# Optimization experiments

Hardware: AMD Instinct MI355X
Metric: run time of the kernel (lower is better)

Reference implementation:

```python
import jax, jax.numpy as jnp
import numpy as np

N_NODES = 50000
N_EDGES = 800000
IN_DIM = 32
HID = 64
OUT_DIM = 4
HEADS = 4
LAYERS = 3
N_GRAPHS = 50
NEG_SLOPE = 0.2
BN_EPS = 1e-5


def setup_inputs() -> dict:
    key = jax.random.key(0)
    ks = jax.random.split(key, 20)
    x = jax.random.normal(ks[0], (N_NODES, IN_DIM), dtype=jnp.float32)
    edge_index = jax.random.randint(ks[1], (2, N_EDGES), 0, N_NODES, dtype=jnp.int64)
    batch = jnp.sort(jax.random.randint(ks[2], (N_NODES,), 0, N_GRAPHS, dtype=jnp.int64))
    s = 0.05
    inp = {
        "x": x,
        "edge_index": edge_index,
        "batch": batch,
        "in_W": jax.random.normal(ks[3], (IN_DIM, HID), jnp.float32) * s,
        "in_b": jnp.zeros((HID,), jnp.float32),
        "gat_W": jax.random.normal(ks[4], (LAYERS, HID, HEADS * HID), jnp.float32) * s,
        "att_src": jax.random.normal(ks[5], (LAYERS, HEADS, HID), jnp.float32) * s,
        "att_dst": jax.random.normal(ks[6], (LAYERS, HEADS, HID), jnp.float32) * s,
        "gat_b": jnp.zeros((LAYERS, HID), jnp.float32),
        "bn_g": jnp.ones((LAYERS, HID), jnp.float32),
        "bn_b": jnp.zeros((LAYERS, HID), jnp.float32),
        "bn_m": jnp.zeros((LAYERS, HID), jnp.float32),
        "bn_v": jnp.ones((LAYERS, HID), jnp.float32),
        "fc1_W": jax.random.normal(ks[7], (HID, HID), jnp.float32) * s,
        "fc1_b": jnp.zeros((HID,), jnp.float32),
        "fc2_W": jax.random.normal(ks[8], (HID, OUT_DIM), jnp.float32) * s,
        "fc2_b": jnp.zeros((OUT_DIM,), jnp.float32),
    }
    return inp


def _gat_layer(x, src, dst, W, a_src, a_dst, b):
    # x: [N, HID]; src/dst: [E'] (self-loops included)
    N = x.shape[0]
    xt = (x @ W).reshape(N, HEADS, HID)           # [N, H, C]
    sc_src = jnp.einsum("nhc,hc->nh", xt, a_src)  # [N, H]
    sc_dst = jnp.einsum("nhc,hc->nh", xt, a_dst)
    e = jax.nn.leaky_relu(sc_src[src] + sc_dst[dst], NEG_SLOPE)  # [E, H]
    # segment softmax over incoming edges of each dst node
    emax = jax.ops.segment_max(e, dst, num_segments=N)
    ex = jnp.exp(e - emax[dst])
    denom = jax.ops.segment_sum(ex, dst, num_segments=N)
    alpha = ex / (denom[dst] + 1e-16)             # [E, H]
    msg = xt[src] * alpha[:, :, None]             # [E, H, C]
    out = jax.ops.segment_sum(msg, dst, num_segments=N)  # [N, H, C]
    return out.mean(axis=1) + b                   # head-average (concat=False)


def reference(x, edge_index, batch, in_W, in_b, gat_W, att_src, att_dst, gat_b,
              bn_g, bn_b, bn_m, bn_v, fc1_W, fc1_b, fc2_W, fc2_b):
    N = x.shape[0]
    loops = jnp.arange(N, dtype=edge_index.dtype)
    src = jnp.concatenate([edge_index[0], loops])
    dst = jnp.concatenate([edge_index[1], loops])

    h = x @ in_W + in_b  # dropout: eval mode (identity)
    for i in range(LAYERS):
        identity = h
        h = _gat_layer(h, src, dst, gat_W[i], att_src[i], att_dst[i], gat_b[i])
        # BatchNorm1d in eval mode (running stats)
        h = (h - bn_m[i]) * jax.lax.rsqrt(bn_v[i] + BN_EPS) * bn_g[i] + bn_b[i]
        h = jax.nn.relu(h)
        h = h + identity

    # global mean pool over graphs
    sums = jax.ops.segment_sum(h, batch, num_segments=N_GRAPHS)
    cnt = jax.ops.segment_sum(jnp.ones((N,), h.dtype), batch, num_segments=N_GRAPHS)
    g = sums / jnp.maximum(cnt, 1.0)[:, None]     # [N_GRAPHS, HID]

    g = jax.nn.relu(g @ fc1_W + fc1_b)
    return g @ fc2_W + fc2_b                      # [N_GRAPHS, OUT_DIM]
```

## Files before the change

### kernel.cpp

```cpp
#include <hip/hip_runtime.h>
#include <hip/hip_fp16.h>
#include <math.h>

#define HID 64
#define HEADS 4
#define HC 256
#define IN_DIM 32
#define NEG 0.2f
#define BN_EPS 1e-5f
#define CAP 64

typedef _Float16 f16;
typedef _Float16 f16x8 __attribute__((ext_vector_type(8)));
typedef float f32x4 __attribute__((ext_vector_type(4)));

__device__ __forceinline__ int ld_idx(const int* __restrict__ p, int i, int f64) {
    return f64 ? p[(size_t)2 * i] : p[i];
}

__global__ void k_init(const int* __restrict__ ei, int* __restrict__ flag,
                       int* __restrict__ deg, float* __restrict__ gsum,
                       int N, int NG) {
    int i = blockIdx.x * blockDim.x + threadIdx.x;
    if (i == 0) {
        int z = 1;
#pragma unroll
        for (int k = 1; k < 64; k += 2) z &= (ei[k] == 0);
        *flag = z;
    }
    if (i < N) deg[i] = 0;
    if (i < NG) gsum[i] = 0.f;
}

__global__ void k_build(const int* __restrict__ ei, const int* __restrict__ flagp,
                        int* __restrict__ deg, unsigned short* __restrict__ src_pad,
                        int E) {
    int e = blockIdx.x * blockDim.x + threadIdx.x;
    if (e >= E) return;
    const int f = *flagp;
    int s = ld_idx(ei, e, f);
    int d = ld_idx(ei, E + e, f);
    int pos = atomicAdd(&deg[d], 1);
    if (pos < CAP) src_pad[(size_t)d * CAP + pos] = (unsigned short)s;
}

__global__ void k_wtilde(const float* __restrict__ gat_W, const float* __restrict__ asrc,
                         const float* __restrict__ adst, float* __restrict__ wts,
                         float* __restrict__ wtd) {
    int l = blockIdx.x;
    int t = threadIdx.x;
    int hh = t >> 6, k = t & 63;
    const float* W = gat_W + (size_t)l * HID * HC + (size_t)k * HC + hh * HID;
    const float* as = asrc + (size_t)l * HEADS * HID + hh * HID;
    const float* ad = adst + (size_t)l * HEADS * HID + hh * HID;
    float s1 = 0.f, s2 = 0.f;
#pragma unroll
    for (int c = 0; c < HID; ++c) { s1 += W[c] * as[c]; s2 += W[c] * ad[c]; }
    wts[l * HC + hh * HID + k] = s1;
    wtd[l * HC + hh * HID + k] = s2;
}

__global__ void k_prepB(const float* __restrict__ gat_W, __half* __restrict__ BT) {
    int l = blockIdx.x;
    int t = threadIdx.x;
    int c = t & 63, jg = t >> 6;
    const float* W = gat_W + (size_t)l * HID * HC;
    __half* o = BT + (size_t)l * HID * HC + (size_t)c * HC + jg * 64;
#pragma unroll
    for (int jj = 0; jj < 64; ++jj)
        o[jj] = __float2half(W[(size_t)jj * HC + jg * 64 + c]);
}

__global__ __launch_bounds__(256) void k_input(
        const float* __restrict__ x, const float* __restrict__ W,
        const float* __restrict__ b, const float* __restrict__ wts0,
        const float* __restrict__ wtd0, float* __restrict__ h,
        __half* __restrict__ h16, float* __restrict__ ssrc,
        float* __restrict__ sdst, int N) {
    int w = threadIdx.x >> 6, lane = threadIdx.x & 63;
    int n = blockIdx.x * 4 + w;
    if (n >= N) return;
    float xv = x[(size_t)n * IN_DIM + (lane & 31)];
    float acc = b[lane];
#pragma unroll
    for (int k = 0; k < IN_DIM; ++k)
        acc += __shfl(xv, k, 64) * W[k * HID + lane];
    h[(size_t)n * HID + lane] = acc;
    h16[(size_t)n * HID + lane] = __float2half(acc);
    float p0 = acc * wts0[0 * HID + lane];
    float p1 = acc * wts0[1 * HID + lane];
    float p2 = acc * wts0[2 * HID + lane];
    float p3 = acc * wts0[3 * HID + lane];
    float q0 = acc * wtd0[0 * HID + lane];
    float q1 = acc * wtd0[1 * HID + lane];
    float q2 = acc * wtd0[2 * HID + lane];
    float q3 = acc * wtd0[3 * HID + lane];
#pragma unroll
    for (int m = 32; m >= 1; m >>= 1) {
        p0 += __shfl_xor(p0, m, 64); p1 += __shfl_xor(p1, m, 64);
        p2 += __shfl_xor(p2, m, 64); p3 += __shfl_xor(p3, m, 64);
        q0 += __shfl_xor(q0, m, 64); q1 += __shfl_xor(q1, m, 64);
        q2 += __shfl_xor(q2, m, 64); q3 += __shfl_xor(q3, m, 64);
    }
    if (lane == 0) {
        *(float4*)(ssrc + (size_t)n * HEADS) = make_float4(p0, p1, p2, p3);
        *(float4*)(sdst + (size_t)n * HEADS) = make_float4(q0, q1, q2, q3);
    }
}

__global__ __launch_bounds__(256) void k_gather(
        const int* __restrict__ deg, const unsigned short* __restrict__ src_pad,
        const float* __restrict__ ssrc, const float* __restrict__ sdst,
        const __half* __restrict__ h16, __half* __restrict__ agg, int N) {
    int d = blockIdx.x * 4 + (threadIdx.x >> 6);
    if (d >= N) return;
    const int lane = threadIdx.x & 63;
    const int g = lane >> 4, l16 = lane & 15;
    const int dg = min(deg[d], CAP);
    const int se = (int)src_pad[(size_t)d * CAP + lane];
    const float4 sdd = *(const float4*)(sdst + (size_t)d * HEADS);
    float den0 = 0.f, den1 = 0.f, den2 = 0.f, den3 = 0.f;
    float a00=0.f,a01=0.f,a02=0.f,a03=0.f, a10=0.f,a11=0.f,a12=0.f,a13=0.f;
    float a20=0.f,a21=0.f,a22=0.f,a23=0.f, a30=0.f,a31=0.f,a32=0.f,a33=0.f;
    {
        float4 ssd = *(const float4*)(ssrc + (size_t)d * HEADS);
        uint2 hu = *(const uint2*)(h16 + (size_t)d * HID + l16 * 4);
        float2 f01 = __half22float2(*(__half2*)&hu.x);
        float2 f23 = __half22float2(*(__half2*)&hu.y);
        if (g == 0) {
            float v0 = ssd.x + sdd.x; v0 = v0 > 0.f ? v0 : NEG * v0;
            float v1 = ssd.y + sdd.y; v1 = v1 > 0.f ? v1 : NEG * v1;
            float v2 = ssd.z + sdd.z; v2 = v2 > 0.f ? v2 : NEG * v2;
            float v3 = ssd.w + sdd.w; v3 = v3 > 0.f ? v3 : NEG * v3;
            float e0 = __expf(v0), e1 = __expf(v1), e2 = __expf(v2), e3 = __expf(v3);
            den0 = e0; den1 = e1; den2 = e2; den3 = e3;
            a00 = e0*f01.x; a01 = e0*f01.y; a02 = e0*f23.x; a03 = e0*f23.y;
            a10 = e1*f01.x; a11 = e1*f01.y; a12 = e1*f23.x; a13 = e1*f23.y;
            a20 = e2*f01.x; a21 = e2*f01.y; a22 = e2*f23.x; a23 = e2*f23.y;
            a30 = e3*f01.x; a31 = e3*f01.y; a32 = e3*f23.x; a33 = e3*f23.y;
        }
    }
    for (int b = 0; b < dg; b += 4) {
        int idx = b + g;
        bool valid = idx < dg;
        int s = __shfl(se, idx, 64);
        s = valid ? s : d;
        float4 ss = *(const float4*)(ssrc + (size_t)s * HEADS);
        uint2 hu = *(const uint2*)(h16 + (size_t)s * HID + l16 * 4);
        float u0 = ss.x + sdd.x; u0 = u0 > 0.f ? u0 : NEG * u0;
        float u1 = ss.y + sdd.y; u1 = u1 > 0.f ? u1 : NEG * u1;
        float u2 = ss.z + sdd.z; u2 = u2 > 0.f ? u2 : NEG * u2;
        float u3 = ss.w + sdd.w; u3 = u3 > 0.f ? u3 : NEG * u3;
        float e0 = valid ? __expf(u0) : 0.f;
        float e1 = valid ? __expf(u1) : 0.f;
        float e2 = valid ? __expf(u2) : 0.f;
        float e3 = valid ? __expf(u3) : 0.f;
        float2 f01 = __half22float2(*(__half2*)&hu.x);
        float2 f23 = __half22float2(*(__half2*)&hu.y);
        den0 += e0; den1 += e1; den2 += e2; den3 += e3;
        a00 += e0*f01.x; a01 += e0*f01.y; a02 += e0*f23.x; a03 += e0*f23.y;
        a10 += e1*f01.x; a11 += e1*f01.y; a12 += e1*f23.x; a13 += e1*f23.y;
        a20 += e2*f01.x; a21 += e2*f01.y; a22 += e2*f23.x; a23 += e2*f23.y;
        a30 += e3*f01.x; a31 += e3*f01.y; a32 += e3*f23.x; a33 += e3*f23.y;
    }
#define FOLD(v) { v += __shfl_xor(v, 16, 64); v += __shfl_xor(v, 32, 64); }
    FOLD(den0) FOLD(den1) FOLD(den2) FOLD(den3)
    FOLD(a00) FOLD(a01) FOLD(a02) FOLD(a03)
    FOLD(a10) FOLD(a11) FOLD(a12) FOLD(a13)
    FOLD(a20) FOLD(a21) FOLD(a22) FOLD(a23)
    FOLD(a30) FOLD(a31) FOLD(a32) FOLD(a33)
#undef FOLD
    float iv, o0, o1, o2, o3;
    if (g == 0)      { iv = 0.25f / den0; o0 = a00; o1 = a01; o2 = a02; o3 = a03; }
    else if (g == 1) { iv = 0.25f / den1; o0 = a10; o1 = a11; o2 = a12; o3 = a13; }
    else if (g == 2) { iv = 0.25f / den2; o0 = a20; o1 = a21; o2 = a22; o3 = a23; }
    else             { iv = 0.25f / den3; o0 = a30; o1 = a31; o2 = a32; o3 = a33; }
    __half2 q01 = __floats2half2_rn(o0 * iv, o1 * iv);
    __half2 q23 = __floats2half2_rn(o2 * iv, o3 * iv);
    uint2 st;
    st.x = *(unsigned int*)&q01;
    st.y = *(unsigned int*)&q23;
    *(uint2*)(agg + ((size_t)d * HC + g * HID + l16 * 4)) = st;
}

__global__ __launch_bounds__(256) void k_postW(
        const __half* __restrict__ agg, const __half* __restrict__ BT,
        const float* __restrict__ gb, const float* __restrict__ bg,
        const float* __restrict__ bb, const float* __restrict__ bm,
        const float* __restrict__ bv, const float* __restrict__ wtsn,
        const float* __restrict__ wtdn, float* __restrict__ h,
        __half* __restrict__ h16, float* __restrict__ ssrc,
        float* __restrict__ sdst, int N) {
    __shared__ float lds[64][68];
    const int t = threadIdx.x;
    const int w = t >> 6, l = t & 63;
    const int l16 = l & 15, lk = l >> 4;
    const f16* BTf = (const f16*)BT;
    const f16* af = (const f16*)agg;
    f16x8 bf[8][4];
#pragma unroll
    for (int ks = 0; ks < 8; ++ks)
#pragma unroll
        for (int nt = 0; nt < 4; ++nt)
            bf[ks][nt] = *(const f16x8*)(BTf + (size_t)(nt * 16 + l16) * HC + ks * 32 + lk * 8);
    int row = blockIdx.x * 64 + w * 16 + l16;
    int rowc = min(row, N - 1);
    f32x4 acc[4];
#pragma unroll
    for (int nt = 0; nt < 4; ++nt) acc[nt] = (f32x4){0.f, 0.f, 0.f, 0.f};
#pragma unroll
    for (int ks = 0; ks < 8; ++ks) {
        f16x8 a = *(const f16x8*)(af + (size_t)rowc * HC + ks * 32 + lk * 8);
#pragma unroll
        for (int nt = 0; nt < 4; ++nt)
            acc[nt] = __builtin_amdgcn_mfma_f32_16x16x32_f16(a, bf[ks][nt], acc[nt], 0, 0, 0);
    }
#pragma unroll
    for (int nt = 0; nt < 4; ++nt)
#pragma unroll
        for (int r = 0; r < 4; ++r)
            lds[w * 16 + lk * 4 + r][nt * 16 + l16] = acc[nt][r];
    __syncthreads();
    {
        int j = t >> 2, q = t & 3;
        int n = blockIdx.x * 64 + j;
        if (n < N) {
            int c0 = q * 16;
            float o[16];
            float* hrow = h + (size_t)n * HID;
#pragma unroll
            for (int i4 = 0; i4 < 4; ++i4) {
                int c = c0 + i4 * 4;
                float4 sv = *(const float4*)&lds[j][c];
                float4 r4 = *(const float4*)(hrow + c);
                float4 gb4 = *(const float4*)(gb + c);
                float4 bg4 = *(const float4*)(bg + c);
                float4 bb4 = *(const float4*)(bb + c);
                float4 bm4 = *(const float4*)(bm + c);
                float4 bv4 = *(const float4*)(bv + c);
                float4 ov;
                float v;
                v = sv.x + gb4.x; v = (v - bm4.x) * rsqrtf(bv4.x + BN_EPS) * bg4.x + bb4.x;
                ov.x = fmaxf(v, 0.f) + r4.x;
                v = sv.y + gb4.y; v = (v - bm4.y) * rsqrtf(bv4.y + BN_EPS) * bg4.y + bb4.y;
                ov.y = fmaxf(v, 0.f) + r4.y;
                v = sv.z + gb4.z; v = (v - bm4.z) * rsqrtf(bv4.z + BN_EPS) * bg4.z + bb4.z;
                ov.z = fmaxf(v, 0.f) + r4.z;
                v = sv.w + gb4.w; v = (v - bm4.w) * rsqrtf(bv4.w + BN_EPS) * bg4.w + bb4.w;
                ov.w = fmaxf(v, 0.f) + r4.w;
                *(float4*)(hrow + c) = ov;
                o[i4 * 4 + 0] = ov.x; o[i4 * 4 + 1] = ov.y;
                o[i4 * 4 + 2] = ov.z; o[i4 * 4 + 3] = ov.w;
            }
            {
                __half2 hp[8];
#pragma unroll
                for (int i = 0; i < 8; ++i)
                    hp[i] = __floats2half2_rn(o[2 * i], o[2 * i + 1]);
                uint4 u0, u1;
                u0.x = *(unsigned*)&hp[0]; u0.y = *(unsigned*)&hp[1];
                u0.z = *(unsigned*)&hp[2]; u0.w = *(unsigned*)&hp[3];
                u1.x = *(unsigned*)&hp[4]; u1.y = *(unsigned*)&hp[5];
                u1.z = *(unsigned*)&hp[6]; u1.w = *(unsigned*)&hp[7];
                *(uint4*)(h16 + (size_t)n * HID + c0) = u0;
                *(uint4*)(h16 + (size_t)n * HID + c0 + 8) = u1;
            }
            if (wtsn) {
                float ps0 = 0.f, ps1 = 0.f, ps2 = 0.f, ps3 = 0.f;
                float pd0 = 0.f, pd1 = 0.f, pd2 = 0.f, pd3 = 0.f;
#pragma unroll
                for (int i = 0; i < 16; ++i) {
                    int c = c0 + i;
                    float ov = o[i];
                    ps0 += ov * wtsn[0 * HID + c]; ps1 += ov * wtsn[1 * HID + c];
                    ps2 += ov * wtsn[2 * HID + c]; ps3 += ov * wtsn[3 * HID + c];
                    pd0 += ov * wtdn[0 * HID + c]; pd1 += ov * wtdn[1 * HID + c];
                    pd2 += ov * wtdn[2 * HID + c]; pd3 += ov * wtdn[3 * HID + c];
                }
#pragma unroll
                for (int m = 2; m >= 1; m >>= 1) {
                    ps0 += __shfl_xor(ps0, m, 64); ps1 += __shfl_xor(ps1, m, 64);
                    ps2 += __shfl_xor(ps2, m, 64); ps3 += __shfl_xor(ps3, m, 64);
                    pd0 += __shfl_xor(pd0, m, 64); pd1 += __shfl_xor(pd1, m, 64);
                    pd2 += __shfl_xor(pd2, m, 64); pd3 += __shfl_xor(pd3, m, 64);
                }
                if (q == 0) {
                    *(float4*)(ssrc + (size_t)n * HEADS) = make_float4(ps0, ps1, ps2, ps3);
                    *(float4*)(sdst + (size_t)n * HEADS) = make_float4(pd0, pd1, pd2, pd3);
                }
            }
        }
    }
}

#define NPBK 64
__global__ void k_pool_sum(const float* __restrict__ h, const int* __restrict__ batch,
                           const int* __restrict__ flagp, float* __restrict__ gsum, int N) {
    const int f = *flagp;
    int c = threadIdx.x;
    int n0 = blockIdx.x * NPBK;
    int n1 = min(n0 + NPBK, N);
    if (n0 >= N) return;
    int cur = ld_idx(batch, n0, f);
    float s = 0.f;
    for (int n = n0; n < n1; ++n) {
        int g = ld_idx(batch, n, f);
        if (g != cur) {
            atomicAdd(&gsum[cur * HID + c], s);
            s = 0.f;
            cur = g;
        }
        s += h[(size_t)n * HID + c];
    }
    atomicAdd(&gsum[cur * HID + c], s);
}

__device__ __forceinline__ int lower_bound_i(const int* __restrict__ a, int n, int v, int f) {
    int lo = 0, hi = n;
    while (lo < hi) {
        int mid = (lo + hi) >> 1;
        if (ld_idx(a, mid, f) < v) lo = mid + 1; else hi = mid;
    }
    return lo;
}

__global__ void k_mlp(const float* __restrict__ gsum, const int* __restrict__ batch,
                      const int* __restrict__ flagp, int N,
                      const float* __restrict__ W1, const float* __restrict__ b1,
                      const float* __restrict__ W2, const float* __restrict__ b2,
                      float* __restrict__ out, int OUTD) {
    int gg = blockIdx.x, c = threadIdx.x;
    const int f = *flagp;
    int lo = lower_bound_i(batch, N, gg, f);
    int hi = lower_bound_i(batch, N, gg + 1, f);
    float cnt = (float)(hi - lo);
    __shared__ float gs[HID];
    __shared__ float s1[HID];
    gs[c] = gsum[gg * HID + c] / fmaxf(cnt, 1.f);
    __syncthreads();
    float acc = b1[c];
#pragma unroll
    for (int k = 0; k < HID; ++k) acc += gs[k] * W1[k * HID + c];
    s1[c] = fmaxf(acc, 0.f);
    __syncthreads();
    if (c < OUTD) {
        float o = b2[c];
#pragma unroll
        for (int k = 0; k < HID; ++k) o += s1[k] * W2[k * OUTD + c];
        out[gg * OUTD + c] = o;
    }
}

extern "C" void kernel_launch(void* const* d_in, const int* in_sizes, int n_in,
                              void* d_out, int out_size, void* d_ws, size_t ws_size,
                              hipStream_t stream) {
    const float* x       = (const float*)d_in[0];
    const int*   ei_raw  = (const int*)d_in[1];
    const int*   b_raw   = (const int*)d_in[2];
    const float* in_W    = (const float*)d_in[3];
    const float* in_b    = (const float*)d_in[4];
    const float* gat_W   = (const float*)d_in[5];
    const float* att_src = (const float*)d_in[6];
    const float* att_dst = (const float*)d_in[7];
    const float* gat_b   = (const float*)d_in[8];
    const float* bn_g    = (const float*)d_in[9];
    const float* bn_b    = (const float*)d_in[10];
    const float* bn_m    = (const float*)d_in[11];
    const float* bn_v    = (const float*)d_in[12];
    const float* fc1_W   = (const float*)d_in[13];
    const float* fc1_b   = (const float*)d_in[14];
    const float* fc2_W   = (const float*)d_in[15];
    const float* fc2_b   = (const float*)d_in[16];

    const int N = in_sizes[2];
    const int E = in_sizes[1] / 2;
    const int OUTD = 4;
    const int G = out_size / OUTD;

    float*  h    = (float*)d_ws;
    __half* h16  = (__half*)(h + (size_t)N * HID);
    __half* agg  = h16 + (size_t)N * HID;
    float*  ssrc = (float*)(agg + (size_t)N * HC);
    float*  sdst = ssrc + (size_t)N * HEADS;
    float*  wts  = sdst + (size_t)N * HEADS;
    float*  wtd  = wts + 3 * HC;
    __half* BT   = (__half*)(wtd + 3 * HC);
    float*  gsum = (float*)(BT + 3 * HID * HC);
    int*    deg  = (int*)(gsum + (size_t)G * HID);
    unsigned short* src_pad = (unsigned short*)(deg + N);
    int*    flag = (int*)(src_pad + (size_t)N * CAP);

    k_init<<<(max(N, G * HID) + 255) / 256, 256, 0, stream>>>(
        ei_raw, flag, deg, gsum, N, G * HID);
    k_build<<<(E + 255) / 256, 256, 0, stream>>>(ei_raw, flag, deg, src_pad, E);
    k_wtilde<<<3, 256, 0, stream>>>(gat_W, att_src, att_dst, wts, wtd);
    k_prepB<<<3, 256, 0, stream>>>(gat_W, BT);
    k_input<<<(N + 3) / 4, 256, 0, stream>>>(x, in_W, in_b, wts, wtd, h, h16,
                                             ssrc, sdst, N);

    for (int l = 0; l < 3; ++l) {
        k_gather<<<(N + 3) / 4, 256, 0, stream>>>(
            deg, src_pad, ssrc, sdst, h16, agg, N);
        const float* wtsn = (l < 2) ? (wts + (l + 1) * HC) : nullptr;
        const float* wtdn = (l < 2) ? (wtd + (l + 1) * HC) : nullptr;
        k_postW<<<(N + 63) / 64, 256, 0, stream>>>(
            agg, BT + (size_t)l * HID * HC,
            gat_b + (size_t)l * HID, bn_g + (size_t)l * HID, bn_b + (size_t)l * HID,
            bn_m + (size_t)l * HID, bn_v + (size_t)l * HID,
            wtsn, wtdn, h, h16, ssrc, sdst, N);
    }

    k_pool_sum<<<(N + NPBK - 1) / NPBK, HID, 0, stream>>>(h, b_raw, flag, gsum, N);
    k_mlp<<<G, HID, 0, stream>>>(gsum, b_raw, flag, N, fc1_W, fc1_b, fc2_W, fc2_b,
                                 (float*)d_out, OUTD);
}
```

Measured before the change: 337.3 us.

## Fold weight prep into init, software-prefetch gather loads, stream B fragments

Merges the attention-weight projection and fp16 B-transpose prep into the init kernel, removing two tiny kernel launches. The gather loop now loads the next edge's source scores and features before computing the current one, which is meant to hide global-memory latency. The post-aggregation GEMM loads B fragments per MFMA instead of holding all 32 in registers. That cuts register pressure and may raise occupancy, at the cost of more repeated loads of B from cache.

After: 328.8 us (median of 2 runs). 1.03x faster.

```diff
diff --git a/kernel.cpp b/kernel.cpp
--- a/kernel.cpp
+++ b/kernel.cpp
@@ -20,7 +20,10 @@
 
 __global__ void k_init(const int* __restrict__ ei, int* __restrict__ flag,
                        int* __restrict__ deg, float* __restrict__ gsum,
-                       int N, int NG) {
+                       int N, int NG,
+                       const float* __restrict__ gat_W, const float* __restrict__ asrc,
+                       const float* __restrict__ adst, float* __restrict__ wts,
+                       float* __restrict__ wtd, __half* __restrict__ BT) {
     int i = blockIdx.x * blockDim.x + threadIdx.x;
     if (i == 0) {
         int z = 1;
@@ -30,6 +33,29 @@
     }
     if (i < N) deg[i] = 0;
     if (i < NG) gsum[i] = 0.f;
+    if (blockIdx.x < 3) {
+        int l = blockIdx.x;
+        int t = threadIdx.x;
+        int hh = t >> 6, k = t & 63;
+        {
+            const float* W = gat_W + (size_t)l * HID * HC + (size_t)k * HC + hh * HID;
+            const float* as = asrc + (size_t)l * HEADS * HID + hh * HID;
+            const float* ad = adst + (size_t)l * HEADS * HID + hh * HID;
+            float s1 = 0.f, s2 = 0.f;
+#pragma unroll
+            for (int c = 0; c < HID; ++c) { s1 += W[c] * as[c]; s2 += W[c] * ad[c]; }
+            wts[l * HC + hh * HID + k] = s1;
+            wtd[l * HC + hh * HID + k] = s2;
+        }
+        {
+            int c = t & 63, jg = t >> 6;
+            const float* W = gat_W + (size_t)l * HID * HC;
+            __half* o = BT + (size_t)l * HID * HC + (size_t)c * HC + jg * 64;
+#pragma unroll
+            for (int jj = 0; jj < 64; ++jj)
+                o[jj] = __float2half(W[(size_t)jj * HC + jg * 64 + c]);
+        }
+    }
 }
 
 __global__ void k_build(const int* __restrict__ ei, const int* __restrict__ flagp,
@@ -42,33 +68,6 @@
     int d = ld_idx(ei, E + e, f);
     int pos = atomicAdd(&deg[d], 1);
     if (pos < CAP) src_pad[(size_t)d * CAP + pos] = (unsigned short)s;
-}
-
-__global__ void k_wtilde(const float* __restrict__ gat_W, const float* __restrict__ asrc,
-                         const float* __restrict__ adst, float* __restrict__ wts,
-                         float* __restrict__ wtd) {
-    int l = blockIdx.x;
-    int t = threadIdx.x;
-    int hh = t >> 6, k = t & 63;
-    const float* W = gat_W + (size_t)l * HID * HC + (size_t)k * HC + hh * HID;
-    const float* as = asrc + (size_t)l * HEADS * HID + hh * HID;
-    const float* ad = adst + (size_t)l * HEADS * HID + hh * HID;
-    float s1 = 0.f, s2 = 0.f;
-#pragma unroll
-    for (int c = 0; c < HID; ++c) { s1 += W[c] * as[c]; s2 += W[c] * ad[c]; }
-    wts[l * HC + hh * HID + k] = s1;
-    wtd[l * HC + hh * HID + k] = s2;
-}
-
-__global__ void k_prepB(const float* __restrict__ gat_W, __half* __restrict__ BT) {
-    int l = blockIdx.x;
-    int t = threadIdx.x;
-    int c = t & 63, jg = t >> 6;
-    const float* W = gat_W + (size_t)l * HID * HC;
-    __half* o = BT + (size_t)l * HID * HC + (size_t)c * HC + jg * 64;
-#pragma unroll
-    for (int jj = 0; jj < 64; ++jj)
-        o[jj] = __float2half(W[(size_t)jj * HC + jg * 64 + c]);
 }
 
 __global__ __launch_bounds__(256) void k_input(
@@ -140,28 +139,32 @@
             a30 = e3*f01.x; a31 = e3*f01.y; a32 = e3*f23.x; a33 = e3*f23.y;
         }
     }
+    bool vc = g < dg;
+    int sc = __shfl(se, g, 64); sc = vc ? sc : d;
+    float4 ss_cur = *(const float4*)(ssrc + (size_t)sc * HEADS);
+    uint2  hu_cur = *(const uint2*)(h16 + (size_t)sc * HID + l16 * 4);
     for (int b = 0; b < dg; b += 4) {
-        int idx = b + g;
-        bool valid = idx < dg;
-        int s = __shfl(se, idx, 64);
-        s = valid ? s : d;
-        float4 ss = *(const float4*)(ssrc + (size_t)s * HEADS);
-        uint2 hu = *(const uint2*)(h16 + (size_t)s * HID + l16 * 4);
-        float u0 = ss.x + sdd.x; u0 = u0 > 0.f ? u0 : NEG * u0;
-        float u1 = ss.y + sdd.y; u1 = u1 > 0.f ? u1 : NEG * u1;
-        float u2 = ss.z + sdd.z; u2 = u2 > 0.f ? u2 : NEG * u2;
-        float u3 = ss.w + sdd.w; u3 = u3 > 0.f ? u3 : NEG * u3;
-        float e0 = valid ? __expf(u0) : 0.f;
-        float e1 = valid ? __expf(u1) : 0.f;
-        float e2 = valid ? __expf(u2) : 0.f;
-        float e3 = valid ? __expf(u3) : 0.f;
-        float2 f01 = __half22float2(*(__half2*)&hu.x);
-        float2 f23 = __half22float2(*(__half2*)&hu.y);
+        int idn = b + 4 + g;
+        bool vn = idn < dg;
+        int sn = __shfl(se, idn & 63, 64); sn = vn ? sn : d;
+        float4 ss_nxt = *(const float4*)(ssrc + (size_t)sn * HEADS);
+        uint2  hu_nxt = *(const uint2*)(h16 + (size_t)sn * HID + l16 * 4);
+        float u0 = ss_cur.x + sdd.x; u0 = u0 > 0.f ? u0 : NEG * u0;
+        float u1 = ss_cur.y + sdd.y; u1 = u1 > 0.f ? u1 : NEG * u1;
+        float u2 = ss_cur.z + sdd.z; u2 = u2 > 0.f ? u2 : NEG * u2;
+        float u3 = ss_cur.w + sdd.w; u3 = u3 > 0.f ? u3 : NEG * u3;
+        float e0 = vc ? __expf(u0) : 0.f;
+        float e1 = vc ? __expf(u1) : 0.f;
+        float e2 = vc ? __expf(u2) : 0.f;
+        float e3 = vc ? __expf(u3) : 0.f;
+        float2 f01 = __half22float2(*(__half2*)&hu_cur.x);
+        float2 f23 = __half22float2(*(__half2*)&hu_cur.y);
         den0 += e0; den1 += e1; den2 += e2; den3 += e3;
         a00 += e0*f01.x; a01 += e0*f01.y; a02 += e0*f23.x; a03 += e0*f23.y;
         a10 += e1*f01.x; a11 += e1*f01.y; a12 += e1*f23.x; a13 += e1*f23.y;
         a20 += e2*f01.x; a21 += e2*f01.y; a22 += e2*f23.x; a23 += e2*f23.y;
         a30 += e3*f01.x; a31 += e3*f01.y; a32 += e3*f23.x; a33 += e3*f23.y;
+        ss_cur = ss_nxt; hu_cur = hu_nxt; vc = vn;
     }
 #define FOLD(v) { v += __shfl_xor(v, 16, 64); v += __shfl_xor(v, 32, 64); }
     FOLD(den0) FOLD(den1) FOLD(den2) FOLD(den3)
@@ -197,12 +200,6 @@
     const int l16 = l & 15, lk = l >> 4;
     const f16* BTf = (const f16*)BT;
     const f16* af = (const f16*)agg;
-    f16x8 bf[8][4];
-#pragma unroll
-    for (int ks = 0; ks < 8; ++ks)
-#pragma unroll
-        for (int nt = 0; nt < 4; ++nt)
-            bf[ks][nt] = *(const f16x8*)(BTf + (size_t)(nt * 16 + l16) * HC + ks * 32 + lk * 8);
     int row = blockIdx.x * 64 + w * 16 + l16;
     int rowc = min(row, N - 1);
     f32x4 acc[4];
@@ -212,8 +209,10 @@
     for (int ks = 0; ks < 8; ++ks) {
         f16x8 a = *(const f16x8*)(af + (size_t)rowc * HC + ks * 32 + lk * 8);
 #pragma unroll
-        for (int nt = 0; nt < 4; ++nt)
-            acc[nt] = __builtin_amdgcn_mfma_f32_16x16x32_f16(a, bf[ks][nt], acc[nt], 0, 0, 0);
+        for (int nt = 0; nt < 4; ++nt) {
+            f16x8 bfr = *(const f16x8*)(BTf + (size_t)(nt * 16 + l16) * HC + ks * 32 + lk * 8);
+            acc[nt] = __builtin_amdgcn_mfma_f32_16x16x32_f16(a, bfr, acc[nt], 0, 0, 0);
+        }
     }
 #pragma unroll
     for (int nt = 0; nt < 4; ++nt)
@@ -391,10 +390,9 @@
     int*    flag = (int*)(src_pad + (size_t)N * CAP);
 
     k_init<<<(max(N, G * HID) + 255) / 256, 256, 0, stream>>>(
-        ei_raw, flag, deg, gsum, N, G * HID);
+        ei_raw, flag, deg, gsum, N, G * HID,
+        gat_W, att_src, att_dst, wts, wtd, BT);
     k_build<<<(E + 255) / 256, 256, 0, stream>>>(ei_raw, flag, deg, src_pad, E);
-    k_wtilde<<<3, 256, 0, stream>>>(gat_W, att_src, att_dst, wts, wtd);
-    k_prepB<<<3, 256, 0, stream>>>(gat_W, BT);
     k_input<<<(N + 3) / 4, 256, 0, stream>>>(x, in_W, in_b, wts, wtd, h, h16,
                                              ssrc, sdst, N);
 
```
